# Kernel tuning notes

Hardware: AMD Instinct MI355X
Metric: run time of the kernel (lower is better)

## Reference

```python
import jax, jax.numpy as jnp
import numpy as np
import math

IN_DIM = 1024
OUT_DIM = 1024
GRID_SIZE = 5
SPLINE_ORDER = 3
N_COEFFS = GRID_SIZE + SPLINE_ORDER          # 8
N_KNOTS = GRID_SIZE + 2 * SPLINE_ORDER + 1   # 12
EPS = 1e-08


def setup_inputs() -> dict:
    key = jax.random.key(0)
    k_x, k_c, k_w = jax.random.split(key, 3)
    B = 4096
    x = jax.random.normal(k_x, (B, IN_DIM), dtype=jnp.float32)
    coeffs = jax.random.normal(k_c, (OUT_DIM, IN_DIM * N_COEFFS), dtype=jnp.float32) * 0.1
    # kaiming_uniform(a=sqrt(5)) -> U(-bound, bound), bound = sqrt(6/((1+a^2)*fan_in)) = 1/sqrt(fan_in)
    bound = 1.0 / math.sqrt(IN_DIM)
    base_weight = jax.random.uniform(k_w, (OUT_DIM, IN_DIM), dtype=jnp.float32,
                                     minval=-bound, maxval=bound)
    step = 2.0 / GRID_SIZE
    init_val = math.log(math.exp(step) - 1.0)
    grid_steps_log = jnp.full((IN_DIM, N_KNOTS - 1), init_val, dtype=jnp.float32)
    grid_start = jnp.full((IN_DIM, 1), -1.0 - SPLINE_ORDER * step, dtype=jnp.float32)
    res_scale = jnp.zeros((1,), dtype=jnp.float32)
    return {"x": x, "coeffs": coeffs, "base_weight": base_weight,
            "grid_steps_log": grid_steps_log, "grid_start": grid_start,
            "res_scale": res_scale}


def _get_grid(grid_steps_log, grid_start):
    steps = jax.nn.softplus(grid_steps_log)            # [in, n_knots-1]
    grid = jnp.concatenate([grid_start, steps], axis=-1)
    return jnp.cumsum(grid, axis=-1)                   # [in, n_knots]


def _b_spline(x, grid):
    # x: [B, in], grid: [in, n_knots] -> bases: [B, in, n_coeffs]
    x_u = x[:, :, None]                                # [B, in, 1]
    g = grid[None, :, :]                               # [1, in, n_knots]
    bases = ((x_u >= g[:, :, :-1]) & (x_u < g[:, :, 1:])).astype(x.dtype)
    for d in range(1, SPLINE_ORDER + 1):
        left = (x_u - g[:, :, :-(d + 1)]) / (g[:, :, d:-1] - g[:, :, :-(d + 1)] + EPS)
        right = (g[:, :, d + 1:] - x_u) / (g[:, :, d + 1:] - g[:, :, 1:-d] + EPS)
        bases = left * bases[:, :, :-1] + right * bases[:, :, 1:]
    return bases


def reference(x, coeffs, base_weight, grid_steps_log, grid_start, res_scale):
    grid = _get_grid(grid_steps_log, grid_start)
    spline_basis = _b_spline(x, grid)                  # [B, in, n_coeffs]
    B = spline_basis.shape[0]
    spline_flat = spline_basis.reshape(B, -1)          # [B, in*n_coeffs]
    spline_out = spline_flat @ coeffs.T                # [B, out]
    base_out = jax.nn.silu(x) @ base_weight.T          # [B, out]
    y = spline_out + base_out
    y = y + res_scale * x                              # residual (in_dim == out_dim)
    return y
```

## Files before the change

### kernel.cpp

```cpp
#include <hip/hip_runtime.h>

#define IN_DIM   1024
#define OUT_DIM  1024
#define BATCH    4096
#define NC       8
#define NK       12
#define KSPLINE  (IN_DIM * NC)
#define KDIM     (KSPLINE + IN_DIM)
#define EPS      1e-8f

#define NBLK_A   ((IN_DIM / 256) * (BATCH / 16))
#define NBLK_W   ((OUT_DIM * (KDIM / 4)) / 256)

#define BM       256
#define BN       256
#define BKQ      32
#define KSPLIT   4
#define KPS      (KDIM / KSPLIT)
#define NKT      (KPS / BKQ)
#define NGBLK    ((BATCH / BM) * (OUT_DIM / BN) * KSPLIT)

#define SWZ(r)   (((r) >> 1) & 3)

typedef _Float16 f16x8  __attribute__((ext_vector_type(8)));
typedef float    f32x4  __attribute__((ext_vector_type(4)));

static __device__ __forceinline__ unsigned short f2h_bits(float f) {
  _Float16 h = (_Float16)f;
  return __builtin_bit_cast(unsigned short, h);
}

static __device__ __forceinline__ void gl_lds16(const unsigned short* g, unsigned short* l) {
  __builtin_amdgcn_global_load_lds(
      (const __attribute__((address_space(1))) unsigned int*)g,
      (__attribute__((address_space(3))) unsigned int*)l, 16, 0, 0);
}

__global__ __launch_bounds__(256) void prep_k(const float* __restrict__ x,
                                              const float* __restrict__ coeffs,
                                              const float* __restrict__ bw,
                                              const float* __restrict__ gsl,
                                              const float* __restrict__ gstart,
                                              const float* __restrict__ rsp,
                                              unsigned short* __restrict__ A,
                                              unsigned short* __restrict__ W,
                                              float* __restrict__ out) {
  const int blk = blockIdx.x;
  if (blk < NBLK_A) {
    const int i  = (blk & 3) * 256 + threadIdx.x;
    const int b0 = (blk >> 2) * 16;
    const float rs = rsp[0];
    float g[NK];
    float acc = gstart[i];
    g[0] = acc;
#pragma unroll
    for (int t = 0; t < NK - 1; ++t) {
      float v  = gsl[i * (NK - 1) + t];
      float sp = (v > 20.f) ? v : log1pf(expf(v));
      acc += sp;
      g[t + 1] = acc;
    }
    float r[30];
#pragma unroll
    for (int j = 0; j < 11; ++j) r[j]      = 1.f / (g[j + 1] - g[j] + EPS);
#pragma unroll
    for (int j = 0; j < 10; ++j) r[11 + j] = 1.f / (g[j + 2] - g[j] + EPS);
#pragma unroll
    for (int j = 0; j <  9; ++j) r[21 + j] = 1.f / (g[j + 3] - g[j] + EPS);

#pragma unroll 4
    for (int bb = 0; bb < 16; ++bb) {
      const int b = b0 + bb;
      float xv = x[(size_t)b * IN_DIM + i];
      float bas[NK - 1];
#pragma unroll
      for (int k = 0; k < NK - 1; ++k)
        bas[k] = (xv >= g[k] && xv < g[k + 1]) ? 1.f : 0.f;
      const int off[3] = {0, 11, 21};
#pragma unroll
      for (int d = 1; d <= 3; ++d) {
#pragma unroll
        for (int k = 0; k < NK - 1 - d; ++k) {
          float left  = (xv - g[k])         * r[off[d - 1] + k];
          float right = (g[k + d + 1] - xv) * r[off[d - 1] + k + 1];
          bas[k] = left * bas[k] + right * bas[k + 1];
        }
      }
      uint4 pack;
      pack.x = (unsigned)f2h_bits(bas[0]) | ((unsigned)f2h_bits(bas[1]) << 16);
      pack.y = (unsigned)f2h_bits(bas[2]) | ((unsigned)f2h_bits(bas[3]) << 16);
      pack.z = (unsigned)f2h_bits(bas[4]) | ((unsigned)f2h_bits(bas[5]) << 16);
      pack.w = (unsigned)f2h_bits(bas[6]) | ((unsigned)f2h_bits(bas[7]) << 16);
      *(uint4*)&A[(size_t)b * KDIM + i * NC] = pack;
      float s = xv / (1.f + expf(-xv));
      A[(size_t)b * KDIM + KSPLINE + i] = f2h_bits(s);
      out[(size_t)b * OUT_DIM + i] = rs * xv;
    }
  } else {
    int idx = (blk - NBLK_A) * 256 + threadIdx.x;
    int n  = idx / (KDIM / 4);
    int k4 = (idx - n * (KDIM / 4)) * 4;
    float4 v;
    if (k4 < KSPLINE) v = *(const float4*)&coeffs[(size_t)n * KSPLINE + k4];
    else              v = *(const float4*)&bw[(size_t)n * IN_DIM + (k4 - KSPLINE)];
    ushort4 o;
    o.x = f2h_bits(v.x); o.y = f2h_bits(v.y); o.z = f2h_bits(v.z); o.w = f2h_bits(v.w);
    *(ushort4*)&W[(size_t)n * KDIM + k4] = o;
  }
}

__global__ __launch_bounds__(512, 1) void gemm_k(const unsigned short* __restrict__ A,
                                                 const unsigned short* __restrict__ W,
                                                 float* __restrict__ out,
                                                 float* __restrict__ P,
                                                 int use_partial) {
  __shared__ __align__(16) unsigned short As[4][BM][BKQ];
  __shared__ __align__(16) unsigned short Bs[4][BN][BKQ];
  const int tid  = threadIdx.x;
  const int wave = tid >> 6;
  const int lane = tid & 63;

  const int s  = (blockIdx.x & 7) * 32 + (blockIdx.x >> 3);
  const int ks = s >> 6;
  const int bn = (s >> 4) & 3;
  const int bm = s & 15;

  const int srow = tid >> 2;
  const int scsw = ((tid & 3) ^ SWZ(srow)) * 8;
  const unsigned short* aG = A + (size_t)(bm * BM + srow) * KDIM + (size_t)ks * KPS + scsw;
  const unsigned short* bG = W + (size_t)(bn * BN + srow) * KDIM + (size_t)ks * KPS + scsw;

#define STAGE(t) do {                                                          \
    const int sl_ = (t) & 3; const int kb_ = (t) * BKQ;                        \
    gl_lds16(aG + kb_,                      &As[sl_][wave * 16][0]);           \
    gl_lds16(aG + (size_t)128 * KDIM + kb_, &As[sl_][128 + wave * 16][0]);     \
    gl_lds16(bG + kb_,                      &Bs[sl_][wave * 16][0]);           \
    gl_lds16(bG + (size_t)128 * KDIM + kb_, &Bs[sl_][128 + wave * 16][0]);     \
  } while (0)

  const int l15 = lane & 15;
  const int kg  = lane >> 4;
  const int wm  = (wave >> 2) * 128;
  const int wn  = (wave & 3) * 64;

  f32x4 acc[8][4] = {};

  STAGE(0); STAGE(1); STAGE(2);
  asm volatile("s_waitcnt vmcnt(8)" ::: "memory");
  __builtin_amdgcn_s_barrier();

#pragma unroll 4
  for (int kt = 0; kt < NKT; ++kt) {
    const unsigned short* as = &As[kt & 3][0][0];
    const unsigned short* bs = &Bs[kt & 3][0][0];
    f16x8 af[8], bf[4];
#pragma unroll
    for (int mt = 0; mt < 8; ++mt) {
      int row = wm + mt * 16 + l15;
      af[mt] = *(const f16x8*)&as[row * BKQ + ((kg ^ SWZ(row)) * 8)];
    }
#pragma unroll
    for (int nt = 0; nt < 4; ++nt) {
      int row = wn + nt * 16 + l15;
      bf[nt] = *(const f16x8*)&bs[row * BKQ + ((kg ^ SWZ(row)) * 8)];
    }
    if (kt < NKT - 3) STAGE(kt + 3);
    __builtin_amdgcn_s_setprio(1);
#pragma unroll
    for (int mt = 0; mt < 8; ++mt)
#pragma unroll
      for (int nt = 0; nt < 4; ++nt)
        acc[mt][nt] = __builtin_amdgcn_mfma_f32_16x16x32_f16(af[mt], bf[nt], acc[mt][nt], 0, 0, 0);
    __builtin_amdgcn_s_setprio(0);
    if (kt < NKT - 3)       asm volatile("s_waitcnt vmcnt(8)" ::: "memory");
    else if (kt == NKT - 3) asm volatile("s_waitcnt vmcnt(4)" ::: "memory");
    else if (kt == NKT - 2) asm volatile("s_waitcnt vmcnt(0)" ::: "memory");
    if (kt < NKT - 1) __builtin_amdgcn_s_barrier();
  }
#undef STAGE

  float* Pk = P + (size_t)(ks - 1) * BATCH * OUT_DIM;
#pragma unroll
  for (int mt = 0; mt < 8; ++mt) {
#pragma unroll
    for (int reg = 0; reg < 4; ++reg) {
      const int row = bm * BM + wm + mt * 16 + kg * 4 + reg;
      const size_t ro = (size_t)row * OUT_DIM;
#pragma unroll
      for (int nt = 0; nt < 4; ++nt) {
        const int col = bn * BN + wn + nt * 16 + l15;
        const float v = acc[mt][nt][reg];
        if (use_partial) {
          if (ks == 0) out[ro + col] += v;
          else         Pk[ro + col]   = v;
        } else {
          atomicAdd(&out[ro + col], v);
        }
      }
    }
  }
}

__global__ __launch_bounds__(256) void reduce_k(float* __restrict__ out,
                                                const float* __restrict__ P) {
  const int n4 = (BATCH * OUT_DIM) / 4;
  const float4* P0 = (const float4*)P;
  const float4* P1 = P0 + n4;
  const float4* P2 = P1 + n4;
  for (int i = blockIdx.x * 256 + threadIdx.x; i < n4; i += gridDim.x * 256) {
    float4 o = ((const float4*)out)[i];
    float4 a = P0[i], b = P1[i], c = P2[i];
    o.x += a.x + b.x + c.x;
    o.y += a.y + b.y + c.y;
    o.z += a.z + b.z + c.z;
    o.w += a.w + b.w + c.w;
    ((float4*)out)[i] = o;
  }
}

extern "C" void kernel_launch(void* const* d_in, const int* in_sizes, int n_in,
                              void* d_out, int out_size, void* d_ws, size_t ws_size,
                              hipStream_t stream) {
  const float* x      = (const float*)d_in[0];
  const float* coeffs = (const float*)d_in[1];
  const float* bw     = (const float*)d_in[2];
  const float* gsl    = (const float*)d_in[3];
  const float* gstart = (const float*)d_in[4];
  const float* rsp    = (const float*)d_in[5];

  const size_t szA = (size_t)BATCH * KDIM * 2;
  const size_t szW = (size_t)OUT_DIM * KDIM * 2;
  const size_t szP = (size_t)BATCH * OUT_DIM * 4 * (KSPLIT - 1);
  char* ws = (char*)d_ws;
  unsigned short* A  = (unsigned short*)ws;
  unsigned short* W  = (unsigned short*)(ws + szA);
  float*          P  = (float*)(ws + szA + szW);
  float*          out = (float*)d_out;
  const int use_partial = (ws_size >= szA + szW + szP) ? 1 : 0;

  prep_k<<<NBLK_A + NBLK_W, 256, 0, stream>>>(x, coeffs, bw, gsl, gstart, rsp, A, W, out);
  gemm_k<<<NGBLK, 512, 0, stream>>>(A, W, out, P, use_partial);
  if (use_partial) reduce_k<<<2048, 256, 0, stream>>>(out, P);
}
```

Measured before the change: 248.2 us.

## Precompute spline grid in separate kernel and retile GEMM to 256x128 with two blocks/CU

Adds a small kernel that computes the knot grid and reciprocal spans once per input feature, so each prep block loads them instead of recomputing softplus, cumsum and divides. SiLU now uses the fast __expf intrinsic. The GEMM changes from 512-thread 256x256 tiles with a 4-stage LDS pipeline to 256-thread 256x128 tiles with double buffering and two blocks per CU. This doubles the grid size, shrinks LDS per block and adds occupancy, at the cost of a shallower prefetch depth, a full vmcnt(0) wait every iteration, and an extra kernel launch.

```diff
diff --git a/kernel.cpp b/kernel.cpp
--- a/kernel.cpp
+++ b/kernel.cpp
@@ -13,7 +13,7 @@
 #define NBLK_W   ((OUT_DIM * (KDIM / 4)) / 256)
 
 #define BM       256
-#define BN       256
+#define BN       128
 #define BKQ      32
 #define KSPLIT   4
 #define KPS      (KDIM / KSPLIT)
@@ -36,11 +36,36 @@
       (__attribute__((address_space(3))) unsigned int*)l, 16, 0, 0);
 }
 
+__global__ __launch_bounds__(256) void grid_k(const float* __restrict__ gsl,
+                                              const float* __restrict__ gstart,
+                                              float* __restrict__ G) {
+  const int i = blockIdx.x * 256 + threadIdx.x;
+  float g[NK];
+  float acc = gstart[i];
+  g[0] = acc;
+#pragma unroll
+  for (int t = 0; t < NK - 1; ++t) {
+    float v  = gsl[i * (NK - 1) + t];
+    float sp = (v > 20.f) ? v : log1pf(expf(v));
+    acc += sp;
+    g[t + 1] = acc;
+  }
+  float* Gi = G + i * 48;
+#pragma unroll
+  for (int j = 0; j < NK; ++j) Gi[j] = g[j];
+#pragma unroll
+  for (int j = 0; j < 11; ++j) Gi[12 + j]      = 1.f / (g[j + 1] - g[j] + EPS);
+#pragma unroll
+  for (int j = 0; j < 10; ++j) Gi[12 + 11 + j] = 1.f / (g[j + 2] - g[j] + EPS);
+#pragma unroll
+  for (int j = 0; j <  9; ++j) Gi[12 + 21 + j] = 1.f / (g[j + 3] - g[j] + EPS);
+  Gi[44] = 0.f; Gi[45] = 0.f; Gi[46] = 0.f; Gi[47] = 0.f;
+}
+
 __global__ __launch_bounds__(256) void prep_k(const float* __restrict__ x,
                                               const float* __restrict__ coeffs,
                                               const float* __restrict__ bw,
-                                              const float* __restrict__ gsl,
-                                              const float* __restrict__ gstart,
+                                              const float* __restrict__ G,
                                               const float* __restrict__ rsp,
                                               unsigned short* __restrict__ A,
                                               unsigned short* __restrict__ W,
@@ -50,23 +75,19 @@
     const int i  = (blk & 3) * 256 + threadIdx.x;
     const int b0 = (blk >> 2) * 16;
     const float rs = rsp[0];
+    const float4* Gi = (const float4*)(G + i * 48);
     float g[NK];
-    float acc = gstart[i];
-    g[0] = acc;
-#pragma unroll
-    for (int t = 0; t < NK - 1; ++t) {
-      float v  = gsl[i * (NK - 1) + t];
-      float sp = (v > 20.f) ? v : log1pf(expf(v));
-      acc += sp;
-      g[t + 1] = acc;
-    }
-    float r[30];
-#pragma unroll
-    for (int j = 0; j < 11; ++j) r[j]      = 1.f / (g[j + 1] - g[j] + EPS);
-#pragma unroll
-    for (int j = 0; j < 10; ++j) r[11 + j] = 1.f / (g[j + 2] - g[j] + EPS);
-#pragma unroll
-    for (int j = 0; j <  9; ++j) r[21 + j] = 1.f / (g[j + 3] - g[j] + EPS);
+    float r[32];
+#pragma unroll
+    for (int j = 0; j < 3; ++j) {
+      float4 v = Gi[j];
+      g[j * 4 + 0] = v.x; g[j * 4 + 1] = v.y; g[j * 4 + 2] = v.z; g[j * 4 + 3] = v.w;
+    }
+#pragma unroll
+    for (int j = 0; j < 8; ++j) {
+      float4 v = Gi[3 + j];
+      r[j * 4 + 0] = v.x; r[j * 4 + 1] = v.y; r[j * 4 + 2] = v.z; r[j * 4 + 3] = v.w;
+    }
 
 #pragma unroll 4
     for (int bb = 0; bb < 16; ++bb) {
@@ -92,7 +113,7 @@
       pack.z = (unsigned)f2h_bits(bas[4]) | ((unsigned)f2h_bits(bas[5]) << 16);
       pack.w = (unsigned)f2h_bits(bas[6]) | ((unsigned)f2h_bits(bas[7]) << 16);
       *(uint4*)&A[(size_t)b * KDIM + i * NC] = pack;
-      float s = xv / (1.f + expf(-xv));
+      float s = xv / (1.f + __expf(-xv));
       A[(size_t)b * KDIM + KSPLINE + i] = f2h_bits(s);
       out[(size_t)b * OUT_DIM + i] = rs * xv;
     }
@@ -109,20 +130,20 @@
   }
 }
 
-__global__ __launch_bounds__(512, 1) void gemm_k(const unsigned short* __restrict__ A,
+__global__ __launch_bounds__(256, 2) void gemm_k(const unsigned short* __restrict__ A,
                                                  const unsigned short* __restrict__ W,
                                                  float* __restrict__ out,
                                                  float* __restrict__ P,
                                                  int use_partial) {
-  __shared__ __align__(16) unsigned short As[4][BM][BKQ];
-  __shared__ __align__(16) unsigned short Bs[4][BN][BKQ];
+  __shared__ __align__(16) unsigned short As[2][BM][BKQ];
+  __shared__ __align__(16) unsigned short Bs[2][BN][BKQ];
   const int tid  = threadIdx.x;
   const int wave = tid >> 6;
   const int lane = tid & 63;
 
-  const int s  = (blockIdx.x & 7) * 32 + (blockIdx.x >> 3);
-  const int ks = s >> 6;
-  const int bn = (s >> 4) & 3;
+  const int s  = (blockIdx.x & 7) * 64 + (blockIdx.x >> 3);
+  const int ks = s >> 7;
+  const int bn = (s >> 4) & 7;
   const int bm = s & 15;
 
   const int srow = tid >> 2;
@@ -131,28 +152,30 @@
   const unsigned short* bG = W + (size_t)(bn * BN + srow) * KDIM + (size_t)ks * KPS + scsw;
 
 #define STAGE(t) do {                                                          \
-    const int sl_ = (t) & 3; const int kb_ = (t) * BKQ;                        \
+    const int sl_ = (t) & 1; const int kb_ = (t) * BKQ;                        \
     gl_lds16(aG + kb_,                      &As[sl_][wave * 16][0]);           \
+    gl_lds16(aG + (size_t) 64 * KDIM + kb_, &As[sl_][ 64 + wave * 16][0]);     \
     gl_lds16(aG + (size_t)128 * KDIM + kb_, &As[sl_][128 + wave * 16][0]);     \
+    gl_lds16(aG + (size_t)192 * KDIM + kb_, &As[sl_][192 + wave * 16][0]);     \
     gl_lds16(bG + kb_,                      &Bs[sl_][wave * 16][0]);           \
-    gl_lds16(bG + (size_t)128 * KDIM + kb_, &Bs[sl_][128 + wave * 16][0]);     \
+    gl_lds16(bG + (size_t) 64 * KDIM + kb_, &Bs[sl_][ 64 + wave * 16][0]);     \
   } while (0)
 
   const int l15 = lane & 15;
   const int kg  = lane >> 4;
-  const int wm  = (wave >> 2) * 128;
-  const int wn  = (wave & 3) * 64;
+  const int wm  = (wave >> 1) * 128;
+  const int wn  = (wave & 1) * 64;
 
   f32x4 acc[8][4] = {};
 
-  STAGE(0); STAGE(1); STAGE(2);
-  asm volatile("s_waitcnt vmcnt(8)" ::: "memory");
+  STAGE(0);
+  asm volatile("s_waitcnt vmcnt(0)" ::: "memory");
   __builtin_amdgcn_s_barrier();
 
-#pragma unroll 4
+#pragma unroll 2
   for (int kt = 0; kt < NKT; ++kt) {
-    const unsigned short* as = &As[kt & 3][0][0];
-    const unsigned short* bs = &Bs[kt & 3][0][0];
+    const unsigned short* as = &As[kt & 1][0][0];
+    const unsigned short* bs = &Bs[kt & 1][0][0];
     f16x8 af[8], bf[4];
 #pragma unroll
     for (int mt = 0; mt < 8; ++mt) {
@@ -164,7 +187,7 @@
       int row = wn + nt * 16 + l15;
       bf[nt] = *(const f16x8*)&bs[row * BKQ + ((kg ^ SWZ(row)) * 8)];
     }
-    if (kt < NKT - 3) STAGE(kt + 3);
+    if (kt < NKT - 1) STAGE(kt + 1);
     __builtin_amdgcn_s_setprio(1);
 #pragma unroll
     for (int mt = 0; mt < 8; ++mt)
@@ -172,10 +195,10 @@
       for (int nt = 0; nt < 4; ++nt)
         acc[mt][nt] = __builtin_amdgcn_mfma_f32_16x16x32_f16(af[mt], bf[nt], acc[mt][nt], 0, 0, 0);
     __builtin_amdgcn_s_setprio(0);
-    if (kt < NKT - 3)       asm volatile("s_waitcnt vmcnt(8)" ::: "memory");
-    else if (kt == NKT - 3) asm volatile("s_waitcnt vmcnt(4)" ::: "memory");
-    else if (kt == NKT - 2) asm volatile("s_waitcnt vmcnt(0)" ::: "memory");
-    if (kt < NKT - 1) __builtin_amdgcn_s_barrier();
+    if (kt < NKT - 1) {
+      asm volatile("s_waitcnt vmcnt(0)" ::: "memory");
+      __builtin_amdgcn_s_barrier();
+    }
   }
 #undef STAGE
 
@@ -230,15 +253,18 @@
 
   const size_t szA = (size_t)BATCH * KDIM * 2;
   const size_t szW = (size_t)OUT_DIM * KDIM * 2;
+  const size_t szG = (size_t)IN_DIM * 48 * 4;
   const size_t szP = (size_t)BATCH * OUT_DIM * 4 * (KSPLIT - 1);
   char* ws = (char*)d_ws;
   unsigned short* A  = (unsigned short*)ws;
   unsigned short* W  = (unsigned short*)(ws + szA);
-  float*          P  = (float*)(ws + szA + szW);
+  float*          G  = (float*)(ws + szA + szW);
+  float*          P  = (float*)(ws + szA + szW + szG);
   float*          out = (float*)d_out;
-  const int use_partial = (ws_size >= szA + szW + szP) ? 1 : 0;
-
-  prep_k<<<NBLK_A + NBLK_W, 256, 0, stream>>>(x, coeffs, bw, gsl, gstart, rsp, A, W, out);
-  gemm_k<<<NGBLK, 512, 0, stream>>>(A, W, out, P, use_partial);
+  const int use_partial = (ws_size >= szA + szW + szG + szP) ? 1 : 0;
+
+  grid_k<<<IN_DIM / 256, 256, 0, stream>>>(gsl, gstart, G);
+  prep_k<<<NBLK_A + NBLK_W, 256, 0, stream>>>(x, coeffs, bw, G, rsp, A, W, out);
+  gemm_k<<<NGBLK, 256, 0, stream>>>(A, W, out, P, use_partial);
   if (use_partial) reduce_k<<<2048, 256, 0, stream>>>(out, P);
 }
```

After: 266.0 us. +7.2%, slower.
